# Optimization experiments

Hardware: AMD Instinct MI355X
Metric: run time of the kernel (lower is better)

The kernel has to match this reference:

```python
import jax, jax.numpy as jnp
import numpy as np

B, NQ, HW, D, H = 4, 100, 4096, 1024, 16
HD = D // H  # head dim = 64
EPS = 1e-5
NEG = -1e9


def layernorm(x, g, b):
    mu = jnp.mean(x, axis=-1, keepdims=True)
    var = jnp.mean(jnp.square(x - mu), axis=-1, keepdims=True)
    return (x - mu) * jax.lax.rsqrt(var + EPS) * g + b


def setup_inputs() -> dict:
    key = jax.random.key(0)
    ks = jax.random.split(key, 6)
    scale = 0.02
    return {
        "q": jax.random.normal(ks[0], (B, NQ, D), dtype=jnp.float32),
        "kv": jax.random.normal(ks[1], (B, HW, D), dtype=jnp.float32),
        "mask": jax.random.randint(ks[2], (B, NQ, HW), 0, 2, dtype=jnp.int32),
        "in_proj_w": scale * jax.random.normal(ks[3], (3 * D, D), dtype=jnp.float32),
        "in_proj_b": jnp.zeros((3 * D,), dtype=jnp.float32),
        "out_w": scale * jax.random.normal(ks[4], (D, D), dtype=jnp.float32),
        "out_b": jnp.zeros((D,), dtype=jnp.float32),
        "g_q": jnp.ones((D,), dtype=jnp.float32),
        "b_q": jnp.zeros((D,), dtype=jnp.float32),
        "g_kv": jnp.ones((D,), dtype=jnp.float32),
        "b_kv": jnp.zeros((D,), dtype=jnp.float32),
    }


def reference(q, kv, mask, in_proj_w, in_proj_b, out_w, out_b, g_q, b_q, g_kv, b_kv):
    qn = layernorm(q, g_q, b_q)      # [B,NQ,D]
    kvn = layernorm(kv, g_kv, b_kv)  # [B,HW,D]

    # nn.MultiheadAttention fused in-projection: rows [Wq; Wk; Wv]
    Wq, Wk, Wv = jnp.split(in_proj_w, 3, axis=0)
    bq, bk, bv = jnp.split(in_proj_b, 3, axis=0)
    qp = (qn @ Wq.T + bq).reshape(B, NQ, H, HD)
    kp = (kvn @ Wk.T + bk).reshape(B, HW, H, HD)
    vp = (kvn @ Wv.T + bv).reshape(B, HW, H, HD)

    scores = jnp.einsum("bqhd,bkhd->bhqk", qp, kp) / jnp.sqrt(jnp.float32(HD))

    # Per-query key mask; a query with an all-zero mask attends everywhere
    # (original code sets key_padding_mask=None when kpm.all()).
    allowed = mask.astype(bool)                                   # [B,NQ,HW]
    has_any = jnp.any(allowed, axis=-1, keepdims=True)
    eff = jnp.where(has_any, allowed, True)
    scores = jnp.where(eff[:, None, :, :], scores, NEG)

    attn = jax.nn.softmax(scores, axis=-1)                        # [B,H,NQ,HW]
    ctx = jnp.einsum("bhqk,bkhd->bqhd", attn, vp).reshape(B, NQ, D)
    return ctx @ out_w.T + out_b
```

## Files before the change

### kernel.cpp

```cpp
#include <hip/hip_runtime.h>
#include <math.h>
#include <stdint.h>

#define B_    4
#define NQ_   100
#define HW_   4096
#define D_    1024
#define H_    16
#define HD_   64
#define NCH_  8
#define KCH_  (HW_/NCH_)
#define QT_   32
#define MP_   512

typedef __attribute__((ext_vector_type(8))) short short8;
typedef __attribute__((ext_vector_type(8))) unsigned short ushort8v;
typedef __attribute__((ext_vector_type(4))) float f32x4;

__device__ __forceinline__ unsigned short f2bf(float f) {
    unsigned int u = __float_as_uint(f);
    u += 0x7fffu + ((u >> 16) & 1u);
    return (unsigned short)(u >> 16);
}
__device__ __forceinline__ float bf2f(unsigned short h) {
    return __uint_as_float(((unsigned int)h) << 16);
}

__device__ __forceinline__ void gl2lds16(const void* g, void* l) {
    typedef __attribute__((address_space(1))) unsigned int gu32;
    typedef __attribute__((address_space(3))) unsigned int lu32;
    __builtin_amdgcn_global_load_lds(
        reinterpret_cast<gu32*>(reinterpret_cast<uintptr_t>(g)),
        reinterpret_cast<lu32*>(reinterpret_cast<uintptr_t>(l)),
        16, 0, 0);
}

#define VMCNT8() asm volatile("s_waitcnt vmcnt(8)" ::: "memory")
#define VMCNT0() asm volatile("s_waitcnt vmcnt(0)" ::: "memory")
#define BARRIER() do { __builtin_amdgcn_s_barrier(); \
                       __builtin_amdgcn_sched_barrier(0); } while (0)

__global__ __launch_bounds__(256) void ln_bf16_kernel(
    const float* __restrict__ x, const float* __restrict__ g,
    const float* __restrict__ be, unsigned short* __restrict__ y, int real_rows)
{
    const int wv = threadIdx.x >> 6, lane = threadIdx.x & 63;
    const int row = blockIdx.x * 4 + wv;
    unsigned short* yr = y + (size_t)row * D_;
    if (row >= real_rows) {
        #pragma unroll
        for (int k = 0; k < 4; ++k)
            *reinterpret_cast<ushort4*>(yr + lane*4 + k*256) = make_ushort4(0,0,0,0);
        return;
    }
    const float* xr = x + (size_t)row * D_;
    float4 v[4];
    float s = 0.f, ss = 0.f;
    #pragma unroll
    for (int k = 0; k < 4; ++k) {
        v[k] = *reinterpret_cast<const float4*>(xr + lane*4 + k*256);
        s  += v[k].x + v[k].y + v[k].z + v[k].w;
        ss += v[k].x*v[k].x + v[k].y*v[k].y + v[k].z*v[k].z + v[k].w*v[k].w;
    }
    #pragma unroll
    for (int o = 1; o < 64; o <<= 1) {
        s  += __shfl_xor(s,  o);
        ss += __shfl_xor(ss, o);
    }
    const float mu = s * (1.0f / D_);
    const float rs = rsqrtf(ss * (1.0f / D_) - mu*mu + 1e-5f);
    #pragma unroll
    for (int k = 0; k < 4; ++k) {
        const float4 gg = *reinterpret_cast<const float4*>(g  + lane*4 + k*256);
        const float4 bb = *reinterpret_cast<const float4*>(be + lane*4 + k*256);
        ushort4 o;
        o.x = f2bf((v[k].x - mu) * rs * gg.x + bb.x);
        o.y = f2bf((v[k].y - mu) * rs * gg.y + bb.y);
        o.z = f2bf((v[k].z - mu) * rs * gg.z + bb.z);
        o.w = f2bf((v[k].w - mu) * rs * gg.w + bb.w);
        *reinterpret_cast<ushort4*>(yr + lane*4 + k*256) = o;
    }
}

__global__ __launch_bounds__(256) void wconv_kernel(
    const float* __restrict__ w, unsigned short* __restrict__ wb)
{
    const int i = blockIdx.x * 256 + threadIdx.x;
    const float4 v = reinterpret_cast<const float4*>(w)[i];
    ushort4 o;
    o.x = f2bf(v.x); o.y = f2bf(v.y); o.z = f2bf(v.z); o.w = f2bf(v.w);
    reinterpret_cast<ushort4*>(wb)[i] = o;
}

__global__ __launch_bounds__(256) void hilo_a_kernel(
    const float* __restrict__ x, unsigned short* __restrict__ y)
{
    const int row = blockIdx.x;
    const int tid = threadIdx.x;
    unsigned short* yr = y + (size_t)row * 3072;
    if (row >= B_*NQ_) {
        const ushort4 z = make_ushort4(0,0,0,0);
        reinterpret_cast<ushort4*>(yr)[tid]        = z;
        reinterpret_cast<ushort4*>(yr + 1024)[tid] = z;
        reinterpret_cast<ushort4*>(yr + 2048)[tid] = z;
        return;
    }
    const float4 v = reinterpret_cast<const float4*>(x + (size_t)row * D_)[tid];
    ushort4 hi, lo;
    hi.x = f2bf(v.x); hi.y = f2bf(v.y); hi.z = f2bf(v.z); hi.w = f2bf(v.w);
    lo.x = f2bf(v.x - bf2f(hi.x)); lo.y = f2bf(v.y - bf2f(hi.y));
    lo.z = f2bf(v.z - bf2f(hi.z)); lo.w = f2bf(v.w - bf2f(hi.w));
    reinterpret_cast<ushort4*>(yr)[tid]        = hi;
    reinterpret_cast<ushort4*>(yr + 1024)[tid] = lo;
    reinterpret_cast<ushort4*>(yr + 2048)[tid] = hi;
}

__global__ __launch_bounds__(256) void hilo_w_kernel(
    const float* __restrict__ w, unsigned short* __restrict__ y)
{
    const int row = blockIdx.x;
    const int tid = threadIdx.x;
    const float4 v = reinterpret_cast<const float4*>(w + (size_t)row * D_)[tid];
    ushort4 hi, lo;
    hi.x = f2bf(v.x); hi.y = f2bf(v.y); hi.z = f2bf(v.z); hi.w = f2bf(v.w);
    lo.x = f2bf(v.x - bf2f(hi.x)); lo.y = f2bf(v.y - bf2f(hi.y));
    lo.z = f2bf(v.z - bf2f(hi.z)); lo.w = f2bf(v.w - bf2f(hi.w));
    unsigned short* yr = y + (size_t)row * 3072;
    reinterpret_cast<ushort4*>(yr)[tid]        = hi;
    reinterpret_cast<ushort4*>(yr + 1024)[tid] = hi;
    reinterpret_cast<ushort4*>(yr + 2048)[tid] = lo;
}

__global__ __launch_bounds__(256) void mpack_kernel(
    const int* __restrict__ mask, unsigned int* __restrict__ mp)
{
    const int qrow = blockIdx.x;
    const int b = blockIdx.y;
    const int tid = threadIdx.x;
    unsigned int word = 0;
    if (qrow < NQ_ && tid < 128) {
        const int4* mr = reinterpret_cast<const int4*>(
            mask + ((size_t)(b*NQ_ + qrow))*HW_ + tid*32);
        #pragma unroll
        for (int j = 0; j < 8; ++j) {
            const int4 v = mr[j];
            word |= (v.x!=0 ? 1u:0u) << (4*j);
            word |= (v.y!=0 ? 1u:0u) << (4*j+1);
            word |= (v.z!=0 ? 1u:0u) << (4*j+2);
            word |= (v.w!=0 ? 1u:0u) << (4*j+3);
        }
    }
    const int wany = __any(word != 0) ? 1 : 0;
    __shared__ int red[4];
    if ((tid & 63) == 0) red[tid >> 6] = wany;
    __syncthreads();
    const int hasany = red[0] | red[1] | red[2] | red[3];
    if (tid < 128)
        mp[((size_t)(b*128 + qrow))*128 + tid] = hasany ? word : 0xFFFFFFFFu;
}

__global__ __launch_bounds__(512, 2) void gemm_kv_kernel(
    const unsigned short* __restrict__ A, const unsigned short* __restrict__ Wb,
    const float* __restrict__ bias, unsigned short* __restrict__ kp,
    unsigned short* __restrict__ vt)
{
    extern __shared__ __align__(16) unsigned short lds[];
    unsigned short* As = lds;
    unsigned short* Bs = lds + 32768;

    const int tid  = threadIdx.x;
    const int wave = tid >> 6;
    const int lane = tid & 63;
    const int lr   = lane & 15, quad = lane >> 4;
    const int wm2  = wave >> 2;
    const int wn4  = wave & 3;

    const int bn = blockIdx.x & 7;
    const int bm = blockIdx.x >> 3;

    const int swz_src = ((lane >> 2) & 3) ^ (lane >> 4);
    const int scol    = ((lane & 3) ^ swz_src) * 8;
    const unsigned short* aSrc0 = A  + (size_t)(bm*256 +       wave*16 + (lane>>2))*D_ + scol;
    const unsigned short* aSrc1 = A  + (size_t)(bm*256 + 128 + wave*16 + (lane>>2))*D_ + scol;
    const unsigned short* bSrc0 = Wb + (size_t)(bn*256 +       wave*16 + (lane>>2))*D_ + scol;
    const unsigned short* bSrc1 = Wb + (size_t)(bn*256 + 128 + wave*16 + (lane>>2))*D_ + scol;
    const int wdst = wave * 512;

    const int kq = (quad ^ (lr & 3) ^ (lr >> 2)) * 8;
    int aoff[8], boff[4];
    #pragma unroll
    for (int fm = 0; fm < 8; ++fm) aoff[fm] = (wm2*128 + fm*16 + lr)*32 + kq;
    #pragma unroll
    for (int fn = 0; fn < 4; ++fn) boff[fn] = (wn4*64  + fn*16 + lr)*32 + kq;

    f32x4 acc[8][4];
    #pragma unroll
    for (int i = 0; i < 8; ++i)
        #pragma unroll
        for (int j = 0; j < 4; ++j)
            acc[i][j] = (f32x4){0.f, 0.f, 0.f, 0.f};

    #pragma unroll
    for (int pt = 0; pt < 3; ++pt) {
        gl2lds16(aSrc0 + pt*32, As + pt*8192 + wdst);
        gl2lds16(aSrc1 + pt*32, As + pt*8192 + 4096 + wdst);
        gl2lds16(bSrc0 + pt*32, Bs + pt*8192 + wdst);
        gl2lds16(bSrc1 + pt*32, Bs + pt*8192 + 4096 + wdst);
    }
    VMCNT8();
    BARRIER();

    #pragma unroll 1
    for (int t = 0; t < 32; ++t) {
        const unsigned short* Asl = As + (t & 3) * 8192;
        const unsigned short* Bsl = Bs + (t & 3) * 8192;
        const int s3 = (t + 3) & 3;
        short8 afr[4], bfr[4];

        #pragma unroll
        for (int fm = 0; fm < 4; ++fm)
            afr[fm] = *reinterpret_cast<const short8*>(&Asl[aoff[fm]]);
        #pragma unroll
        for (int fn = 0; fn < 4; ++fn)
            bfr[fn] = *reinterpret_cast<const short8*>(&Bsl[boff[fn]]);
        if (t < 29) {
            gl2lds16(aSrc0 + (t+3)*32, As + s3*8192 + wdst);
            gl2lds16(aSrc1 + (t+3)*32, As + s3*8192 + 4096 + wdst);
        }
        BARRIER();
        __builtin_amdgcn_s_setprio(1);
        #pragma unroll
        for (int fm = 0; fm < 4; ++fm)
            #pragma unroll
            for (int fn = 0; fn < 4; ++fn)
                acc[fm][fn] = __builtin_amdgcn_mfma_f32_16x16x32_bf16(
                    afr[fm], bfr[fn], acc[fm][fn], 0, 0, 0);
        __builtin_amdgcn_s_setprio(0);
        BARRIER();

        #pragma unroll
        for (int fm = 0; fm < 4; ++fm)
            afr[fm] = *reinterpret_cast<const short8*>(&Asl[aoff[fm + 4]]);
        if (t < 29) {
            gl2lds16(bSrc0 + (t+3)*32, Bs + s3*8192 + wdst);
            gl2lds16(bSrc1 + (t+3)*32, Bs + s3*8192 + 4096 + wdst);
        }
        BARRIER();
        __builtin_amdgcn_s_setprio(1);
        #pragma unroll
        for (int fm = 0; fm < 4; ++fm)
            #pragma unroll
            for (int fn = 0; fn < 4; ++fn)
                acc[fm + 4][fn] = __builtin_amdgcn_mfma_f32_16x16x32_bf16(
                    afr[fm], bfr[fn], acc[fm + 4][fn], 0, 0, 0);
        __builtin_amdgcn_s_setprio(0);
        if (t < 29)      { VMCNT8(); }
        else if (t < 31) { VMCNT0(); }
        BARRIER();
    }

    const int colbase = bn*256 + wn4*64 + lr;
    const int mbase   = bm*256 + wm2*128 + quad*4;
    if (bn < 4) {
        #pragma unroll
        for (int fn = 0; fn < 4; ++fn) {
            const int n = colbase + fn*16;
            const float bb = bias[n];
            #pragma unroll
            for (int fm = 0; fm < 8; ++fm) {
                unsigned short* Cp = kp + (size_t)(mbase + fm*16)*1024 + n;
                #pragma unroll
                for (int r = 0; r < 4; ++r)
                    Cp[(size_t)r * 1024] = f2bf(acc[fm][fn][r] + bb);
            }
        }
    } else {
        const int b = bm >> 4;
        const int key0 = mbase - b*4096;
        #pragma unroll
        for (int fn = 0; fn < 4; ++fn) {
            const int n = colbase + fn*16;
            const float bb = bias[n];
            unsigned short* vrow = vt + (size_t)(b*1024 + n - 1024) * HW_;
            #pragma unroll
            for (int fm = 0; fm < 8; ++fm) {
                ushort4 o;
                o.x = f2bf(acc[fm][fn][0] + bb);
                o.y = f2bf(acc[fm][fn][1] + bb);
                o.z = f2bf(acc[fm][fn][2] + bb);
                o.w = f2bf(acc[fm][fn][3] + bb);
                *reinterpret_cast<ushort4*>(vrow + key0 + fm*16) = o;
            }
        }
    }
}

__global__ __launch_bounds__(256) void gemm_splitk_kernel(
    const unsigned short* __restrict__ A, const unsigned short* __restrict__ W,
    float* __restrict__ P, int K, int KS)
{
    __shared__ __align__(16) unsigned short As[2048];
    __shared__ __align__(16) unsigned short Bs[2048];
    const int tid = threadIdx.x;
    const int wave = tid >> 6, lane = tid & 63;
    const int lr = lane & 15, quad = lane >> 4;
    const int bn = blockIdx.x, bm = blockIdx.y, sk = blockIdx.z;

    const int r0 = tid >> 2;
    const int xs = (r0 & 3) ^ ((r0 >> 2) & 3);
    const int kc = (tid & 3) ^ xs;
    const unsigned short* ap = A + (size_t)(bm*64 + r0)*K + sk*KS + kc*8;
    const unsigned short* bp = W + (size_t)(bn*64 + r0)*K + sk*KS + kc*8;
    unsigned short* asd = As + wave*512;
    unsigned short* bsd = Bs + wave*512;

    f32x4 acc[4];
    #pragma unroll
    for (int j = 0; j < 4; ++j) acc[j] = (f32x4){0.f,0.f,0.f,0.f};

    const int arow = wave*16 + lr;
    const int xa = (arow & 3) ^ ((arow >> 2) & 3);
    const int aoff = (arow*4 + (quad ^ xa))*8;
    int boff[4];
    #pragma unroll
    for (int j = 0; j < 4; ++j) {
        const int brow = j*16 + lr;
        const int xb = (brow & 3) ^ ((brow >> 2) & 3);
        boff[j] = (brow*4 + (quad ^ xb))*8;
    }

    const int nsteps = KS >> 5;
    for (int s = 0; s < nsteps; ++s) {
        gl2lds16(ap, asd); gl2lds16(bp, bsd);
        ap += 32; bp += 32;
        __syncthreads();
        const short8 af = *reinterpret_cast<const short8*>(&As[aoff]);
        short8 bf[4];
        #pragma unroll
        for (int j = 0; j < 4; ++j)
            bf[j] = *reinterpret_cast<const short8*>(&Bs[boff[j]]);
        #pragma unroll
        for (int j = 0; j < 4; ++j)
            acc[j] = __builtin_amdgcn_mfma_f32_16x16x32_bf16(af, bf[j], acc[j], 0, 0, 0);
        __syncthreads();
    }

    float* Pb = P + ((size_t)sk*MP_ + bm*64)*1024 + bn*64;
    const int m0 = wave*16 + quad*4;
    #pragma unroll
    for (int j = 0; j < 4; ++j)
        #pragma unroll
        for (int r = 0; r < 4; ++r)
            Pb[(size_t)(m0 + r)*1024 + j*16 + lr] = acc[j][r];
}

__global__ __launch_bounds__(256) void reduce_kernel(
    const float* __restrict__ P, const float* __restrict__ bias,
    float* __restrict__ Cout, int SK)
{
    const int i4 = blockIdx.x * 256 + threadIdx.x;
    const int c4 = i4 & 255;
    float4 s = reinterpret_cast<const float4*>(bias)[c4];
    for (int sk = 0; sk < SK; ++sk) {
        const float4 p = reinterpret_cast<const float4*>(P + (size_t)sk*MP_*1024)[i4];
        s.x += p.x; s.y += p.y; s.z += p.z; s.w += p.w;
    }
    reinterpret_cast<float4*>(Cout)[i4] = s;
}

__global__ __launch_bounds__(256) void flash_kernel(
    const float* __restrict__ qp, const unsigned short* __restrict__ kp,
    const unsigned short* __restrict__ vt, const unsigned int* __restrict__ mpack,
    float* __restrict__ partO, float* __restrict__ partL)
{
    __shared__ __align__(16) unsigned char smem[49152];
    unsigned short* Ks  = (unsigned short*)smem;
    unsigned short* Vts = (unsigned short*)(smem + 16384);
    unsigned short* Qs  = (unsigned short*)(smem + 32768);
    unsigned short* Ps  = (unsigned short*)(smem + 37376);
    unsigned int*   MWs = (unsigned int*)  (smem + 47616);
    float*          mlW = (float*)         (smem + 48128);
    float*          Om  = (float*)smem;

    const int tid = threadIdx.x;
    const int wave = tid >> 6, lane = tid & 63;
    const int lr = lane & 15, quad = lane >> 4;
    const int qt = blockIdx.x, h = blockIdx.y;
    const int b = blockIdx.z >> 3, ks = blockIdx.z & 7;
    const int kb0 = ks * KCH_;

    {
        const int q = tid >> 3, dc = (tid & 7) * 8;
        const int qg = qt*QT_ + q;
        float4 v0 = make_float4(0.f,0.f,0.f,0.f), v1 = v0;
        if (qg < NQ_) {
            const float* src = qp + ((size_t)(b*NQ_ + qg))*D_ + h*HD_ + dc;
            v0 = *reinterpret_cast<const float4*>(src);
            v1 = *reinterpret_cast<const float4*>(src + 4);
        }
        ushort8v o;
        o[0]=f2bf(v0.x*0.125f); o[1]=f2bf(v0.y*0.125f);
        o[2]=f2bf(v0.z*0.125f); o[3]=f2bf(v0.w*0.125f);
        o[4]=f2bf(v1.x*0.125f); o[5]=f2bf(v1.y*0.125f);
        o[6]=f2bf(v1.z*0.125f); o[7]=f2bf(v1.w*0.125f);
        *reinterpret_cast<ushort8v*>(&Qs[q*72 + dc]) = o;
    }

    const unsigned short* kptr[4];
    const unsigned short* vptr[4];
    #pragma unroll
    for (int i = 0; i < 4; ++i) {
        const int s = i*256 + tid;
        const int key = s >> 3, jg = (s & 7) ^ (key & 7);
        kptr[i] = kp + ((size_t)(b*HW_) + kb0 + key)*1024 + h*HD_ + jg*8;
        const int d = s >> 4, js = s & 15, jg2 = js ^ (d & 15);
        vptr[i] = vt + ((size_t)(b*1024 + h*HD_ + d))*HW_ + kb0 + jg2*8;
    }

    int koff[2][2], voff[4];
    #pragma unroll
    for (int kj = 0; kj < 2; ++kj)
        #pragma unroll
        for (int ds = 0; ds < 2; ++ds) {
            const int key_l = wave*32 + kj*16 + lr;
            const int jg = ds*4 + quad;
            koff[kj][ds] = (key_l*8 + (jg ^ (key_l & 7))) * 8;
        }
    #pragma unroll
    for (int dj = 0; dj < 4; ++dj) {
        const int d_l = dj*16 + lr;
        const int jg = wave*4 + quad;
        voff[dj] = (d_l*16 + (jg ^ (d_l & 15))) * 8;
    }

    float lreg[8];
    #pragma unroll
    for (int i = 0; i < 8; ++i) lreg[i] = 0.f;
    f32x4 Ov[2][4];
    #pragma unroll
    for (int i = 0; i < 2; ++i)
        #pragma unroll
        for (int j = 0; j < 4; ++j)
            Ov[i][j] = (f32x4){0.f,0.f,0.f,0.f};

    for (int kt = 0; kt < 4; ++kt) {
        __syncthreads();
        #pragma unroll
        for (int i = 0; i < 4; ++i) {
            gl2lds16(kptr[i], Ks  + (i*256 + wave*64)*8);
            gl2lds16(vptr[i], Vts + (i*256 + wave*64)*8);
            kptr[i] += 128*1024; vptr[i] += 128;
        }
        if (tid < 128) {
            const int mw = tid >> 5, mq = tid & 31;
            MWs[mw*32 + mq] = mpack[((size_t)(b*128 + qt*QT_ + mq))*128 +
                                    (ks*16 + kt*4 + mw)];
        }
        __syncthreads();

        f32x4 S[2][2];
        #pragma unroll
        for (int i = 0; i < 2; ++i)
            #pragma unroll
            for (int kj = 0; kj < 2; ++kj)
                S[i][kj] = (f32x4){0.f,0.f,0.f,0.f};
        #pragma unroll
        for (int ds = 0; ds < 2; ++ds) {
            short8 aq[2], bk[2];
            aq[0] = *reinterpret_cast<const short8*>(&Qs[(     lr)*72 + ds*32 + quad*8]);
            aq[1] = *reinterpret_cast<const short8*>(&Qs[(16 + lr)*72 + ds*32 + quad*8]);
            bk[0] = *reinterpret_cast<const short8*>(&Ks[koff[0][ds]]);
            bk[1] = *reinterpret_cast<const short8*>(&Ks[koff[1][ds]]);
            #pragma unroll
            for (int i = 0; i < 2; ++i)
                #pragma unroll
                for (int kj = 0; kj < 2; ++kj)
                    S[i][kj] = __builtin_amdgcn_mfma_f32_16x16x32_bf16(
                        aq[i], bk[kj], S[i][kj], 0, 0, 0);
        }

        #pragma unroll
        for (int i = 0; i < 2; ++i) {
            #pragma unroll
            for (int r = 0; r < 4; ++r) {
                const int q = i*16 + quad*4 + r;
                const unsigned int mw = MWs[wave*32 + q];
                const float p0 = ((mw >> lr) & 1u)        ? __expf(S[i][0][r]) : 0.f;
                const float p1 = ((mw >> (16 + lr)) & 1u) ? __expf(S[i][1][r]) : 0.f;
                lreg[i*4+r] += p0 + p1;
                const float p0n = __shfl_xor(p0, 1);
                const float p1n = __shfl_xor(p1, 1);
                if (!(lr & 1)) {
                    const unsigned int w0 = (unsigned)f2bf(p0) | ((unsigned)f2bf(p0n) << 16);
                    const unsigned int w1 = (unsigned)f2bf(p1) | ((unsigned)f2bf(p1n) << 16);
                    *reinterpret_cast<unsigned int*>(&Ps[wave*1280 + q*40 + lr])      = w0;
                    *reinterpret_cast<unsigned int*>(&Ps[wave*1280 + q*40 + 16 + lr]) = w1;
                }
            }
        }

        short8 pf[2], vf[4];
        #pragma unroll
        for (int i = 0; i < 2; ++i)
            pf[i] = *reinterpret_cast<const short8*>(&Ps[wave*1280 + (i*16+lr)*40 + quad*8]);
        #pragma unroll
        for (int dj = 0; dj < 4; ++dj)
            vf[dj] = *reinterpret_cast<const short8*>(&Vts[voff[dj]]);
        #pragma unroll
        for (int i = 0; i < 2; ++i)
            #pragma unroll
            for (int dj = 0; dj < 4; ++dj)
                Ov[i][dj] = __builtin_amdgcn_mfma_f32_16x16x32_bf16(
                    pf[i], vf[dj], Ov[i][dj], 0, 0, 0);
    }

    __syncthreads();
    #pragma unroll
    for (int i = 0; i < 2; ++i)
        #pragma unroll
        for (int r = 0; r < 4; ++r) {
            float l = lreg[i*4+r];
            #pragma unroll
            for (int o = 1; o < 16; o <<= 1) l += __shfl_xor(l, o);
            if (lr == 0) mlW[wave*32 + i*16 + quad*4 + r] = l;
        }
    #pragma unroll
    for (int i = 0; i < 2; ++i)
        #pragma unroll
        for (int dj = 0; dj < 4; ++dj)
            #pragma unroll
            for (int r = 0; r < 4; ++r) {
                const int q = i*16 + quad*4 + r;
                Om[wave*2112 + q*66 + dj*16 + lr] = Ov[i][dj][r];
            }
    __syncthreads();
    {
        const int q = tid >> 3, dc = (tid & 7) * 8;
        float L = 0.f;
        #pragma unroll
        for (int w = 0; w < 4; ++w) L += mlW[w*32 + q];
        float os[8] = {};
        #pragma unroll
        for (int w = 0; w < 4; ++w)
            #pragma unroll
            for (int j = 0; j < 8; ++j)
                os[j] += Om[w*2112 + q*66 + dc + j];
        const size_t pr = (((size_t)(b*H_ + h))*NCH_ + ks)*128 + qt*QT_ + q;
        *reinterpret_cast<float4*>(&partO[pr*HD_ + dc])     = make_float4(os[0],os[1],os[2],os[3]);
        *reinterpret_cast<float4*>(&partO[pr*HD_ + dc + 4]) = make_float4(os[4],os[5],os[6],os[7]);
        if ((tid & 7) == 0) partL[pr] = L;
    }
}

__global__ __launch_bounds__(64) void combine_kernel(
    const float* __restrict__ partO, const float* __restrict__ partL,
    float* __restrict__ ctx)
{
    const int d = threadIdx.x;
    const int qi = blockIdx.x, h = blockIdx.y, b = blockIdx.z;
    const size_t base = ((size_t)(b*H_ + h)) * NCH_ * 128;
    float L = 0.f, O = 0.f;
    #pragma unroll
    for (int i = 0; i < NCH_; ++i) {
        const size_t r = base + i*128 + qi;
        L += partL[r];
        O += partO[r*HD_ + d];
    }
    ctx[((size_t)(b*NQ_ + qi))*D_ + h*HD_ + d] = O / L;
}

extern "C" void kernel_launch(void* const* d_in, const int* in_sizes, int n_in,
                              void* d_out, int out_size, void* d_ws, size_t ws_size,
                              hipStream_t stream)
{
    const float* q     = (const float*)d_in[0];
    const float* kv    = (const float*)d_in[1];
    const int*   mask  = (const int*)  d_in[2];
    const float* in_w  = (const float*)d_in[3];
    const float* in_b  = (const float*)d_in[4];
    const float* out_w = (const float*)d_in[5];
    const float* out_b = (const float*)d_in[6];
    const float* g_q   = (const float*)d_in[7];
    const float* b_q   = (const float*)d_in[8];
    const float* g_kv  = (const float*)d_in[9];
    const float* b_kv  = (const float*)d_in[10];
    float* out = (float*)d_out;

    char* ws = (char*)d_ws;
    float*          qp       = (float*)         (ws + 0);
    unsigned int*   mpackp   = (unsigned int*)  (ws + 1638400);
    unsigned short* wfull_bf = (unsigned short*)(ws + 1900544);
    unsigned short* qn_bf    = (unsigned short*)(ws + 8192000);
    unsigned short* ctx_cat  = (unsigned short*)(ws + 9240576);
    unsigned short* wout_cat = (unsigned short*)(ws + 12386304);
    float*          P        = (float*)         (ws + 18677760);
    float*          ctx      = (float*)         (ws + 35454976);
    float*          partL    = (float*)         (ws + 37093376);
    float*          partO    = (float*)         (ws + 37355520);
    unsigned short* kvn_bf   = (unsigned short*)(ws + 54132736);
    unsigned short* kp       = (unsigned short*)(ws + 87687168);
    unsigned short* vt       = (unsigned short*)(ws + 121241600);

    static bool attr_set = false;
    if (!attr_set) {
        hipFuncSetAttribute(reinterpret_cast<const void*>(gemm_kv_kernel),
                            hipFuncAttributeMaxDynamicSharedMemorySize, 131072);
        attr_set = true;
    }

    mpack_kernel<<<dim3(128, B_), 256, 0, stream>>>(mask, mpackp);
    wconv_kernel<<<3*D_*D_/4/256, 256, 0, stream>>>(in_w, wfull_bf);
    ln_bf16_kernel<<<B_*HW_/4, 256, 0, stream>>>(kv, g_kv, b_kv, kvn_bf, B_*HW_);
    ln_bf16_kernel<<<MP_/4, 256, 0, stream>>>(q, g_q, b_q, qn_bf, B_*NQ_);

    gemm_splitk_kernel<<<dim3(D_/64, MP_/64, 8), 256, 0, stream>>>(
        qn_bf, wfull_bf, P, D_, 128);
    reduce_kernel<<<B_*NQ_*D_/4/256, 256, 0, stream>>>(P, in_b, qp, 8);

    gemm_kv_kernel<<<512, 512, 131072, stream>>>(
        kvn_bf, wfull_bf + (size_t)D_*D_, in_b + D_, kp, vt);

    flash_kernel<<<dim3(4, H_, B_*NCH_), 256, 0, stream>>>(
        qp, kp, vt, mpackp, partO, partL);
    combine_kernel<<<dim3(NQ_, H_, B_), 64, 0, stream>>>(partO, partL, ctx);

    hilo_a_kernel<<<MP_, 256, 0, stream>>>(ctx, ctx_cat);
    hilo_w_kernel<<<D_, 256, 0, stream>>>(out_w, wout_cat);
    gemm_splitk_kernel<<<dim3(D_/64, MP_/64, 8), 256, 0, stream>>>(
        ctx_cat, wout_cat, P, 3*D_, 384);
    reduce_kernel<<<B_*NQ_*D_/4/256, 256, 0, stream>>>(P, out_b, out, 8);
}
```

Before: 327.1 us.

## Shrink KV GEMM tile to 256x128 with triple-buffered LDS and fewer barriers

The K/V projection GEMM now uses 256x128 output tiles instead of 256x256, which doubles the grid to 1024 blocks. Its LDS pipeline goes from four stages to three, cutting shared memory from 128 KB to 72 KB, and launch bounds now ask for four blocks per CU. The intra-iteration barriers are removed, leaving one barrier per k-step, and the wait counts are retuned. The aim is higher occupancy, better load balance and less sync overhead. In exchange, B-tile reuse per block drops and there are fewer accumulators per wave, so each block issues more global loads per FLOP.

Measured after the change: 314.2 us. 1.04x faster.

```diff
diff --git a/kernel.cpp b/kernel.cpp
--- a/kernel.cpp
+++ b/kernel.cpp
@@ -35,7 +35,7 @@
         16, 0, 0);
 }
 
-#define VMCNT8() asm volatile("s_waitcnt vmcnt(8)" ::: "memory")
+#define VMCNT3() asm volatile("s_waitcnt vmcnt(3)" ::: "memory")
 #define VMCNT0() asm volatile("s_waitcnt vmcnt(0)" ::: "memory")
 #define BARRIER() do { __builtin_amdgcn_s_barrier(); \
                        __builtin_amdgcn_sched_barrier(0); } while (0)
@@ -159,14 +159,12 @@
         mp[((size_t)(b*128 + qrow))*128 + tid] = hasany ? word : 0xFFFFFFFFu;
 }
 
-__global__ __launch_bounds__(512, 2) void gemm_kv_kernel(
+__global__ __launch_bounds__(512, 4) void gemm_kv_kernel(
     const unsigned short* __restrict__ A, const unsigned short* __restrict__ Wb,
     const float* __restrict__ bias, unsigned short* __restrict__ kp,
     unsigned short* __restrict__ vt)
 {
     extern __shared__ __align__(16) unsigned short lds[];
-    unsigned short* As = lds;
-    unsigned short* Bs = lds + 32768;
 
     const int tid  = threadIdx.x;
     const int wave = tid >> 6;
@@ -175,95 +173,99 @@
     const int wm2  = wave >> 2;
     const int wn4  = wave & 3;
 
-    const int bn = blockIdx.x & 7;
-    const int bm = blockIdx.x >> 3;
-
-    const int swz_src = ((lane >> 2) & 3) ^ (lane >> 4);
-    const int scol    = ((lane & 3) ^ swz_src) * 8;
-    const unsigned short* aSrc0 = A  + (size_t)(bm*256 +       wave*16 + (lane>>2))*D_ + scol;
-    const unsigned short* aSrc1 = A  + (size_t)(bm*256 + 128 + wave*16 + (lane>>2))*D_ + scol;
-    const unsigned short* bSrc0 = Wb + (size_t)(bn*256 +       wave*16 + (lane>>2))*D_ + scol;
-    const unsigned short* bSrc1 = Wb + (size_t)(bn*256 + 128 + wave*16 + (lane>>2))*D_ + scol;
+    const int bn = blockIdx.x & 15;
+    const int bm = blockIdx.x >> 4;
+
+    const int srow = tid >> 2;
+    const int sswz = (srow & 3) ^ ((srow >> 2) & 3);
+    const int scol = ((tid & 3) ^ sswz) * 8;
+    const unsigned short* aSrc0 = A  + (size_t)(bm*256 + srow      )*D_ + scol;
+    const unsigned short* aSrc1 = A  + (size_t)(bm*256 + srow + 128)*D_ + scol;
+    const unsigned short* bSrc  = Wb + (size_t)(bn*128 + srow      )*D_ + scol;
     const int wdst = wave * 512;
 
-    const int kq = (quad ^ (lr & 3) ^ (lr >> 2)) * 8;
-    int aoff[8], boff[4];
-    #pragma unroll
-    for (int fm = 0; fm < 8; ++fm) aoff[fm] = (wm2*128 + fm*16 + lr)*32 + kq;
-    #pragma unroll
-    for (int fn = 0; fn < 4; ++fn) boff[fn] = (wn4*64  + fn*16 + lr)*32 + kq;
-
-    f32x4 acc[8][4];
+    int aoff[8], boff[2];
+    #pragma unroll
+    for (int fm = 0; fm < 8; ++fm) {
+        const int row = wm2*128 + fm*16 + lr;
+        aoff[fm] = row*32 + (quad ^ (row & 3) ^ ((row >> 2) & 3))*8;
+    }
+    #pragma unroll
+    for (int fn = 0; fn < 2; ++fn) {
+        const int row = wn4*32 + fn*16 + lr;
+        boff[fn] = 8192 + row*32 + (quad ^ (row & 3) ^ ((row >> 2) & 3))*8;
+    }
+
+    f32x4 acc[8][2];
     #pragma unroll
     for (int i = 0; i < 8; ++i)
         #pragma unroll
-        for (int j = 0; j < 4; ++j)
+        for (int j = 0; j < 2; ++j)
             acc[i][j] = (f32x4){0.f, 0.f, 0.f, 0.f};
 
     #pragma unroll
-    for (int pt = 0; pt < 3; ++pt) {
-        gl2lds16(aSrc0 + pt*32, As + pt*8192 + wdst);
-        gl2lds16(aSrc1 + pt*32, As + pt*8192 + 4096 + wdst);
-        gl2lds16(bSrc0 + pt*32, Bs + pt*8192 + wdst);
-        gl2lds16(bSrc1 + pt*32, Bs + pt*8192 + 4096 + wdst);
-    }
-    VMCNT8();
+    for (int pt = 0; pt < 2; ++pt) {
+        gl2lds16(aSrc0 + pt*32, lds + pt*12288 +        wdst);
+        gl2lds16(aSrc1 + pt*32, lds + pt*12288 + 4096 + wdst);
+        gl2lds16(bSrc  + pt*32, lds + pt*12288 + 8192 + wdst);
+    }
+    aSrc0 += 64; aSrc1 += 64; bSrc += 64;
+    VMCNT3();
     BARRIER();
 
+    int cur = 0, nx2 = 2;
     #pragma unroll 1
     for (int t = 0; t < 32; ++t) {
-        const unsigned short* Asl = As + (t & 3) * 8192;
-        const unsigned short* Bsl = Bs + (t & 3) * 8192;
-        const int s3 = (t + 3) & 3;
-        short8 afr[4], bfr[4];
+        const unsigned short* Sl = lds + cur*12288;
+        unsigned short*       S2 = lds + nx2*12288;
+        short8 afr[4], bfr[2];
 
         #pragma unroll
         for (int fm = 0; fm < 4; ++fm)
-            afr[fm] = *reinterpret_cast<const short8*>(&Asl[aoff[fm]]);
-        #pragma unroll
-        for (int fn = 0; fn < 4; ++fn)
-            bfr[fn] = *reinterpret_cast<const short8*>(&Bsl[boff[fn]]);
-        if (t < 29) {
-            gl2lds16(aSrc0 + (t+3)*32, As + s3*8192 + wdst);
-            gl2lds16(aSrc1 + (t+3)*32, As + s3*8192 + 4096 + wdst);
-        }
-        BARRIER();
+            afr[fm] = *reinterpret_cast<const short8*>(&Sl[aoff[fm]]);
+        bfr[0] = *reinterpret_cast<const short8*>(&Sl[boff[0]]);
+        bfr[1] = *reinterpret_cast<const short8*>(&Sl[boff[1]]);
+        if (t < 30) {
+            gl2lds16(aSrc0, S2 +        wdst);
+            gl2lds16(aSrc1, S2 + 4096 + wdst);
+        }
         __builtin_amdgcn_s_setprio(1);
         #pragma unroll
         for (int fm = 0; fm < 4; ++fm)
             #pragma unroll
-            for (int fn = 0; fn < 4; ++fn)
+            for (int fn = 0; fn < 2; ++fn)
                 acc[fm][fn] = __builtin_amdgcn_mfma_f32_16x16x32_bf16(
                     afr[fm], bfr[fn], acc[fm][fn], 0, 0, 0);
         __builtin_amdgcn_s_setprio(0);
-        BARRIER();
 
         #pragma unroll
         for (int fm = 0; fm < 4; ++fm)
-            afr[fm] = *reinterpret_cast<const short8*>(&Asl[aoff[fm + 4]]);
-        if (t < 29) {
-            gl2lds16(bSrc0 + (t+3)*32, Bs + s3*8192 + wdst);
-            gl2lds16(bSrc1 + (t+3)*32, Bs + s3*8192 + 4096 + wdst);
-        }
-        BARRIER();
+            afr[fm] = *reinterpret_cast<const short8*>(&Sl[aoff[fm + 4]]);
+        if (t < 30) {
+            gl2lds16(bSrc, S2 + 8192 + wdst);
+            aSrc0 += 32; aSrc1 += 32; bSrc += 32;
+        }
         __builtin_amdgcn_s_setprio(1);
         #pragma unroll
         for (int fm = 0; fm < 4; ++fm)
             #pragma unroll
-            for (int fn = 0; fn < 4; ++fn)
+            for (int fn = 0; fn < 2; ++fn)
                 acc[fm + 4][fn] = __builtin_amdgcn_mfma_f32_16x16x32_bf16(
                     afr[fm], bfr[fn], acc[fm + 4][fn], 0, 0, 0);
         __builtin_amdgcn_s_setprio(0);
-        if (t < 29)      { VMCNT8(); }
-        else if (t < 31) { VMCNT0(); }
+
+        if (t < 30)       { VMCNT3(); }
+        else if (t == 30) { VMCNT0(); }
         BARRIER();
-    }
-
-    const int colbase = bn*256 + wn4*64 + lr;
+        cur = (cur == 2) ? 0 : cur + 1;
+        nx2 = (nx2 == 2) ? 0 : nx2 + 1;
+    }
+
+    const int colbase = bn*128 + wn4*32 + lr;
     const int mbase   = bm*256 + wm2*128 + quad*4;
-    if (bn < 4) {
-        #pragma unroll
-        for (int fn = 0; fn < 4; ++fn) {
+    if (bn < 8) {
+        #pragma unroll
+        for (int fn = 0; fn < 2; ++fn) {
             const int n = colbase + fn*16;
             const float bb = bias[n];
             #pragma unroll
@@ -278,7 +280,7 @@
         const int b = bm >> 4;
         const int key0 = mbase - b*4096;
         #pragma unroll
-        for (int fn = 0; fn < 4; ++fn) {
+        for (int fn = 0; fn < 2; ++fn) {
             const int n = colbase + fn*16;
             const float bb = bias[n];
             unsigned short* vrow = vt + (size_t)(b*1024 + n - 1024) * HW_;
@@ -604,7 +606,7 @@
     static bool attr_set = false;
     if (!attr_set) {
         hipFuncSetAttribute(reinterpret_cast<const void*>(gemm_kv_kernel),
-                            hipFuncAttributeMaxDynamicSharedMemorySize, 131072);
+                            hipFuncAttributeMaxDynamicSharedMemorySize, 73728);
         attr_set = true;
     }
 
@@ -617,7 +619,7 @@
         qn_bf, wfull_bf, P, D_, 128);
     reduce_kernel<<<B_*NQ_*D_/4/256, 256, 0, stream>>>(P, in_b, qp, 8);
 
-    gemm_kv_kernel<<<512, 512, 131072, stream>>>(
+    gemm_kv_kernel<<<dim3(1024), 512, 73728, stream>>>(
         kvn_bf, wfull_bf + (size_t)D_*D_, in_b + D_, kp, vt);
 
     flash_kernel<<<dim3(4, H_, B_*NCH_), 256, 0, stream>>>(
```
